# Kernel tuning notes

Hardware: AMD Instinct MI355X
Metric: run time of the kernel (lower is better)

## Reference

```python
import jax, jax.numpy as jnp
import numpy as np

FEATS = 64
H = FEATS * FEATS            # GRU hidden size = 4096
I = (FEATS + 1) * FEATS * 3  # GRU input size = 12480


def setup_inputs() -> dict:
    key = jax.random.key(0)
    ks = jax.random.split(key, 16)
    s = 0.02
    inp = {
        "data": jax.random.normal(ks[0], (FEATS, FEATS), dtype=jnp.float32),
        "hidden": jax.random.normal(ks[1], (1, 1, H), dtype=jnp.float32),
        # feature GAT params: fc (in=FEATS -> heads*out=FEATS*1, no fc bias in DGL GATConv)
        "fgat_W": jax.random.normal(ks[2], (FEATS, FEATS), dtype=jnp.float32) * s,
        "fgat_al": jax.random.normal(ks[3], (FEATS,), dtype=jnp.float32) * s,
        "fgat_ar": jax.random.normal(ks[4], (FEATS,), dtype=jnp.float32) * s,
        "fgat_b": jnp.zeros((FEATS,), dtype=jnp.float32),
        # time GAT params
        "tgat_W": jax.random.normal(ks[5], (FEATS, FEATS), dtype=jnp.float32) * s,
        "tgat_al": jax.random.normal(ks[6], (FEATS,), dtype=jnp.float32) * s,
        "tgat_ar": jax.random.normal(ks[7], (FEATS,), dtype=jnp.float32) * s,
        "tgat_b": jnp.zeros((FEATS,), dtype=jnp.float32),
        # GRU params (PyTorch layout: gates stacked [r, z, n])
        "W_ih": jax.random.normal(ks[8], (3 * H, I), dtype=jnp.float32) * s,
        "W_hh": jax.random.normal(ks[9], (3 * H, H), dtype=jnp.float32) * s,
        "b_ih": jnp.zeros((3 * H,), dtype=jnp.float32),
        "b_hh": jnp.zeros((3 * H,), dtype=jnp.float32),
    }
    return inp


def _gat_star(x, W, al, ar, b):
    """DGL GATConv(in=F, out=1, heads=F) on the star graph:
    edges src=1..F -> dst=0, plus self-loops on every node.
    x: (F+1, F). Returns (F+1, F) (out_feats=1 squeezed into head dim)."""
    h = x @ W                      # (N, heads) since out_feats == 1
    el = h * al                    # src attention logits per head
    er = h * ar                    # dst attention logits per head
    # Node 0 receives edges from every node (incl. its self-loop):
    e = jax.nn.leaky_relu(el + er[0], negative_slope=0.2)  # (N, heads)
    alpha = jax.nn.softmax(e, axis=0)
    out0 = jnp.sum(alpha * h, axis=0)                       # (heads,)
    # Nodes 1..F only have their self-loop -> softmax weight 1 -> out = h[v]
    out = h.at[0].set(out0) + b
    return out


def reference(data, hidden, fgat_W, fgat_al, fgat_ar, fgat_b,
              tgat_W, tgat_al, tgat_ar, tgat_b,
              W_ih, W_hh, b_ih, b_hh):
    F = FEATS
    d = data.reshape(F, F)
    zrow = jnp.zeros((1, F), dtype=d.dtype)

    data_r = jnp.concatenate([zrow, d], axis=0)        # (F+1, F)
    feat_r = _gat_star(data_r, fgat_W, fgat_al, fgat_ar, fgat_b)   # (F+1, F)

    data_t = jnp.concatenate([zrow, d.T], axis=0)      # (F+1, F)
    time_r = _gat_star(data_t, tgat_W, tgat_al, tgat_ar, tgat_b)   # (F+1, F)

    dd = data_r[..., None]                              # (F+1, F, 1)
    x = jnp.concatenate([dd, feat_r[..., None], time_r[..., None]], axis=2)
    x = x.reshape(-1)                                   # ((F+1)*F*3,)

    # single-step GRU (PyTorch gate math)
    h0 = hidden.reshape(-1)                             # (H,)
    gi = W_ih @ x + b_ih                                # (3H,)
    gh = W_hh @ h0 + b_hh                               # (3H,)
    r = jax.nn.sigmoid(gi[:H] + gh[:H])
    z = jax.nn.sigmoid(gi[H:2 * H] + gh[H:2 * H])
    n = jnp.tanh(gi[2 * H:] + r * gh[2 * H:])
    h_new = (1.0 - z) * n + z * h0                      # (H,)

    return (h_new, h_new.reshape(1, 1, H))
```

## Files before the change

### kernel.cpp

```cpp
#include <hip/hip_runtime.h>

#define FEATS 64
#define HSZ   4096
#define ISZ   12480
#define I4    (ISZ/4)
#define H4    (HSZ/4)

#define X_OFF  0
#define GI_OFF 12480
#define GH_OFF 24768

#define GI_RPW 4
#define GI_RPB 16
#define GH_RPW 12
#define GH_RPB 48
#define GI_NB  (3 * HSZ / GI_RPB)
#define GH_NB  (3 * HSZ / GH_RPB)

typedef float f4 __attribute__((ext_vector_type(4)));

__global__ __launch_bounds__(256)
void gat_fused(const float* __restrict__ data,
               const float* __restrict__ fW, const float* __restrict__ fal,
               const float* __restrict__ fb,
               const float* __restrict__ tW, const float* __restrict__ tal,
               const float* __restrict__ tb,
               float* __restrict__ ws) {
    __shared__ float ld[64][65];
    __shared__ float Wl[64][65];
    __shared__ float hb[64][65];
    __shared__ float out0[64];
    int w   = blockIdx.x;
    int tid = threadIdx.x;
    const float* W  = w ? tW  : fW;
    const float* al = w ? tal : fal;
    const float* bb = w ? tb  : fb;

    for (int i = tid; i < 4096; i += 256) {
        int r = i >> 6, c = i & 63;
        float v = data[i];
        if (w) ld[c][r] = v; else ld[r][c] = v;
        Wl[r][c] = W[i];
    }
    __syncthreads();

    {
        int vbase = (tid >> 6) * 16;
        int j     = tid & 63;
        float acc[16];
        #pragma unroll
        for (int v = 0; v < 16; ++v) acc[v] = 0.f;
        for (int k = 0; k < 64; ++k) {
            float wk = Wl[k][j];
            #pragma unroll
            for (int v = 0; v < 16; ++v)
                acc[v] = fmaf(ld[vbase + v][k], wk, acc[v]);
        }
        #pragma unroll
        for (int v = 0; v < 16; ++v) hb[vbase + v][j] = acc[v];
    }
    __syncthreads();

    if (tid < 64) {
        int j = tid;
        float a = al[j];
        float m = 0.f;
        for (int v = 0; v < 64; ++v) {
            float e = hb[v][j] * a;
            e = e > 0.f ? e : 0.2f * e;
            m = fmaxf(m, e);
        }
        float sum = __expf(0.f - m);
        float num = 0.f;
        for (int v = 0; v < 64; ++v) {
            float hv = hb[v][j];
            float e  = hv * a;
            e = e > 0.f ? e : 0.2f * e;
            float p  = __expf(e - m);
            sum += p;
            num += p * hv;
        }
        out0[j] = num / sum;
    }
    __syncthreads();

    for (int i = tid; i < 4160; i += 256) {
        int n = i >> 6, f = i & 63;
        float val = ((n == 0) ? out0[f] : hb[n - 1][f]) + bb[f];
        ws[X_OFF + i * 3 + 1 + w] = val;
        if (w == 0)
            ws[X_OFF + i * 3] = (n == 0) ? 0.f : data[(n - 1) * 64 + f];
    }
}

__device__ __forceinline__ float wave_reduce(float v) {
    #pragma unroll
    for (int off = 32; off > 0; off >>= 1) v += __shfl_down(v, off);
    return v;
}

__device__ __forceinline__ float fma4(f4 w, f4 v, float a) {
    return fmaf(w.x, v.x, fmaf(w.y, v.y, fmaf(w.z, v.z, fmaf(w.w, v.w, a))));
}

__device__ __forceinline__ f4 ntload(const f4* p) {
    return __builtin_nontemporal_load(p);
}

__global__ __launch_bounds__(256, 4)
void big_matvec(const float* __restrict__ W_ih,
                const float* __restrict__ W_hh,
                const float* __restrict__ h0,
                float* __restrict__ ws) {
    int b    = blockIdx.x;
    int wave = threadIdx.x >> 6;
    int lane = threadIdx.x & 63;

    if (b < GI_NB) {
        int r = b * GI_RPB + wave * GI_RPW;
        const f4* x4 = (const f4*)(ws + X_OFF);
        const f4* W0 = (const f4*)W_ih + (size_t)r * I4;
        const f4* W1 = W0 + I4;
        const f4* W2 = W1 + I4;
        const f4* W3 = W2 + I4;
        float a0 = 0.f, a1 = 0.f, a2 = 0.f, a3 = 0.f;
        int k = lane;
        #pragma unroll 4
        for (int i = 0; i < 48; ++i, k += 64) {
            f4 v = x4[k];
            a0 = fma4(ntload(W0 + k), v, a0);
            a1 = fma4(ntload(W1 + k), v, a1);
            a2 = fma4(ntload(W2 + k), v, a2);
            a3 = fma4(ntload(W3 + k), v, a3);
        }
        if (lane < 48) {
            int kk = 3072 + lane;
            f4 v = x4[kk];
            a0 = fma4(ntload(W0 + kk), v, a0);
            a1 = fma4(ntload(W1 + kk), v, a1);
            a2 = fma4(ntload(W2 + kk), v, a2);
            a3 = fma4(ntload(W3 + kk), v, a3);
        }
        a0 = wave_reduce(a0);
        a1 = wave_reduce(a1);
        a2 = wave_reduce(a2);
        a3 = wave_reduce(a3);
        if (lane == 0) {
            ws[GI_OFF + r]     = a0;
            ws[GI_OFF + r + 1] = a1;
            ws[GI_OFF + r + 2] = a2;
            ws[GI_OFF + r + 3] = a3;
        }
    } else {
        int base = (b - GI_NB) * GH_RPB + wave * GH_RPW;
        const f4* h4 = (const f4*)h0;
        #pragma unroll
        for (int p = 0; p < GH_RPW; p += 4) {
            int r = base + p;
            const f4* W0 = (const f4*)W_hh + (size_t)r * H4;
            const f4* W1 = W0 + H4;
            const f4* W2 = W1 + H4;
            const f4* W3 = W2 + H4;
            float a0 = 0.f, a1 = 0.f, a2 = 0.f, a3 = 0.f;
            int k = lane;
            #pragma unroll 4
            for (int i = 0; i < 16; ++i, k += 64) {
                f4 v = h4[k];
                a0 = fma4(ntload(W0 + k), v, a0);
                a1 = fma4(ntload(W1 + k), v, a1);
                a2 = fma4(ntload(W2 + k), v, a2);
                a3 = fma4(ntload(W3 + k), v, a3);
            }
            a0 = wave_reduce(a0);
            a1 = wave_reduce(a1);
            a2 = wave_reduce(a2);
            a3 = wave_reduce(a3);
            if (lane == 0) {
                ws[GH_OFF + r]     = a0;
                ws[GH_OFF + r + 1] = a1;
                ws[GH_OFF + r + 2] = a2;
                ws[GH_OFF + r + 3] = a3;
            }
        }
    }
}

__global__ void gru_combine(const float* __restrict__ h0,
                            const float* __restrict__ b_ih,
                            const float* __restrict__ b_hh,
                            const float* __restrict__ ws,
                            float* __restrict__ out) {
    int j = blockIdx.x * 256 + threadIdx.x;
    if (j >= HSZ) return;
    const float* gi = ws + GI_OFF;
    const float* gh = ws + GH_OFF;
    float ir  = gi[j]         + b_ih[j];
    float iz  = gi[HSZ + j]   + b_ih[HSZ + j];
    float in_ = gi[2*HSZ + j] + b_ih[2*HSZ + j];
    float hr  = gh[j]         + b_hh[j];
    float hz  = gh[HSZ + j]   + b_hh[HSZ + j];
    float hn  = gh[2*HSZ + j] + b_hh[2*HSZ + j];
    float r = 1.f / (1.f + expf(-(ir + hr)));
    float z = 1.f / (1.f + expf(-(iz + hz)));
    float n = tanhf(in_ + r * hn);
    float h = (1.f - z) * n + z * h0[j];
    out[j]       = h;
    out[HSZ + j] = h;
}

extern "C" void kernel_launch(void* const* d_in, const int* in_sizes, int n_in,
                              void* d_out, int out_size, void* d_ws, size_t ws_size,
                              hipStream_t stream) {
    const float* data    = (const float*)d_in[0];
    const float* hidden  = (const float*)d_in[1];
    const float* fgat_W  = (const float*)d_in[2];
    const float* fgat_al = (const float*)d_in[3];
    const float* fgat_b  = (const float*)d_in[5];
    const float* tgat_W  = (const float*)d_in[6];
    const float* tgat_al = (const float*)d_in[7];
    const float* tgat_b  = (const float*)d_in[9];
    const float* W_ih    = (const float*)d_in[10];
    const float* W_hh    = (const float*)d_in[11];
    const float* b_ih    = (const float*)d_in[12];
    const float* b_hh    = (const float*)d_in[13];
    float* ws  = (float*)d_ws;
    float* out = (float*)d_out;

    gat_fused<<<2, 256, 0, stream>>>(data, fgat_W, fgat_al, fgat_b,
                                     tgat_W, tgat_al, tgat_b, ws);
    big_matvec<<<GI_NB + GH_NB, 256, 0, stream>>>(W_ih, W_hh, hidden, ws);
    gru_combine<<<HSZ / 256, 256, 0, stream>>>(hidden, b_ih, b_hh, ws, out);
}
```

Baseline: 140.7 us.

## Fuse GAT, GRU matvecs and gate combine into one persistent kernel

Merges the three launches into a single 512-block kernel. Blocks 0-1 compute the GAT features and signal completion through an atomic counter, and every block computes its W_hh rows while that work runs. Each block then spins until x is ready, computes its W_ih rows, and the last block to finish (found with a second atomic) applies the GRU gate math. This removes launch gaps and overlaps the small GAT stage with the W_hh streaming. The cost is a memset launch, a spin-wait whose safety depends on blocks 0-1 being resident, and a serial combine done by only one block.

Measured after the change: 279.4 us. 98.6% more time.

```diff
diff --git a/kernel.cpp b/kernel.cpp
--- a/kernel.cpp
+++ b/kernel.cpp
@@ -6,206 +6,206 @@
 #define I4    (ISZ/4)
 #define H4    (HSZ/4)
 
-#define X_OFF  0
-#define GI_OFF 12480
-#define GH_OFF 24768
-
-#define GI_RPW 4
-#define GI_RPB 16
-#define GH_RPW 12
-#define GH_RPB 48
-#define GI_NB  (3 * HSZ / GI_RPB)
-#define GH_NB  (3 * HSZ / GH_RPB)
+#define X_OFF   0
+#define GI_OFF  12480
+#define GH_OFF  24768
+#define SYNC_OFF 37056
+
+#define NBLK 512
+#define RPB  24
+#define RPW  6
 
 typedef float f4 __attribute__((ext_vector_type(4)));
 
-__global__ __launch_bounds__(256)
-void gat_fused(const float* __restrict__ data,
-               const float* __restrict__ fW, const float* __restrict__ fal,
-               const float* __restrict__ fb,
-               const float* __restrict__ tW, const float* __restrict__ tal,
-               const float* __restrict__ tb,
-               float* __restrict__ ws) {
-    __shared__ float ld[64][65];
-    __shared__ float Wl[64][65];
+__device__ __forceinline__ float wave_reduce(float v) {
+    #pragma unroll
+    for (int off = 32; off > 0; off >>= 1) v += __shfl_down(v, off);
+    return v;
+}
+
+__device__ __forceinline__ float fma4(f4 w, f4 v, float a) {
+    return fmaf(w.x, v.x, fmaf(w.y, v.y, fmaf(w.z, v.z, fmaf(w.w, v.w, a))));
+}
+
+__device__ __forceinline__ f4 ntload(const f4* p) {
+    return __builtin_nontemporal_load(p);
+}
+
+__global__ __launch_bounds__(256, 2)
+void mega(const float* __restrict__ data,
+          const float* __restrict__ fW, const float* __restrict__ fal,
+          const float* __restrict__ fb,
+          const float* __restrict__ tW, const float* __restrict__ tal,
+          const float* __restrict__ tb,
+          const float* __restrict__ W_ih, const float* __restrict__ W_hh,
+          const float* __restrict__ h0,
+          const float* __restrict__ b_ih, const float* __restrict__ b_hh,
+          float* __restrict__ ws, float* __restrict__ out) {
     __shared__ float hb[64][65];
     __shared__ float out0[64];
-    int w   = blockIdx.x;
-    int tid = threadIdx.x;
-    const float* W  = w ? tW  : fW;
-    const float* al = w ? tal : fal;
-    const float* bb = w ? tb  : fb;
-
-    for (int i = tid; i < 4096; i += 256) {
-        int r = i >> 6, c = i & 63;
-        float v = data[i];
-        if (w) ld[c][r] = v; else ld[r][c] = v;
-        Wl[r][c] = W[i];
-    }
-    __syncthreads();
-
-    {
-        int vbase = (tid >> 6) * 16;
-        int j     = tid & 63;
+    __shared__ int   sLast;
+    int b = blockIdx.x, tid = threadIdx.x;
+    int wave = tid >> 6, lane = tid & 63;
+    int* sync = (int*)(ws + SYNC_OFF);
+
+    if (b < 2) {
+        const float* Wg = b ? tW  : fW;
+        const float* al = b ? tal : fal;
+        const float* bb = b ? tb  : fb;
+        int vbase = wave * 16, j = lane;
         float acc[16];
         #pragma unroll
         for (int v = 0; v < 16; ++v) acc[v] = 0.f;
         for (int k = 0; k < 64; ++k) {
-            float wk = Wl[k][j];
+            float wk = Wg[k * 64 + j];
             #pragma unroll
-            for (int v = 0; v < 16; ++v)
-                acc[v] = fmaf(ld[vbase + v][k], wk, acc[v]);
+            for (int v = 0; v < 16; ++v) {
+                float dv = b ? data[k * 64 + vbase + v]
+                             : data[(vbase + v) * 64 + k];
+                acc[v] = fmaf(dv, wk, acc[v]);
+            }
         }
         #pragma unroll
         for (int v = 0; v < 16; ++v) hb[vbase + v][j] = acc[v];
+        __syncthreads();
+
+        if (tid < 64) {
+            int j2 = tid;
+            float a = al[j2];
+            float m = 0.f;
+            for (int v = 0; v < 64; ++v) {
+                float e = hb[v][j2] * a;
+                e = e > 0.f ? e : 0.2f * e;
+                m = fmaxf(m, e);
+            }
+            float sum = __expf(0.f - m);
+            float num = 0.f;
+            for (int v = 0; v < 64; ++v) {
+                float hv = hb[v][j2];
+                float e  = hv * a;
+                e = e > 0.f ? e : 0.2f * e;
+                float p  = __expf(e - m);
+                sum += p;
+                num += p * hv;
+            }
+            out0[j2] = num / sum;
+        }
+        __syncthreads();
+
+        for (int i = tid; i < 4160; i += 256) {
+            int n = i >> 6, f = i & 63;
+            float val = ((n == 0) ? out0[f] : hb[n - 1][f]) + bb[f];
+            ws[X_OFF + i * 3 + 1 + b] = val;
+            if (b == 0)
+                ws[X_OFF + i * 3] = (n == 0) ? 0.f : data[(n - 1) * 64 + f];
+        }
+        __syncthreads();
+        __threadfence();
+        if (tid == 0)
+            __hip_atomic_fetch_add(sync, 1, __ATOMIC_RELEASE,
+                                   __HIP_MEMORY_SCOPE_AGENT);
+    }
+
+    {
+        int r = b * RPB + wave * RPW;
+        const f4* h4 = (const f4*)h0;
+        const f4* Wb = (const f4*)W_hh + (size_t)r * H4;
+        float a0 = 0.f, a1 = 0.f, a2 = 0.f, a3 = 0.f, a4 = 0.f, a5 = 0.f;
+        int k = lane;
+        #pragma unroll 2
+        for (int i = 0; i < 16; ++i, k += 64) {
+            f4 v = h4[k];
+            a0 = fma4(ntload(Wb + k),          v, a0);
+            a1 = fma4(ntload(Wb + H4 + k),     v, a1);
+            a2 = fma4(ntload(Wb + 2 * H4 + k), v, a2);
+            a3 = fma4(ntload(Wb + 3 * H4 + k), v, a3);
+            a4 = fma4(ntload(Wb + 4 * H4 + k), v, a4);
+            a5 = fma4(ntload(Wb + 5 * H4 + k), v, a5);
+        }
+        a0 = wave_reduce(a0); a1 = wave_reduce(a1); a2 = wave_reduce(a2);
+        a3 = wave_reduce(a3); a4 = wave_reduce(a4); a5 = wave_reduce(a5);
+        if (lane == 0) {
+            ws[GH_OFF + r]     = a0 + b_hh[r];
+            ws[GH_OFF + r + 1] = a1 + b_hh[r + 1];
+            ws[GH_OFF + r + 2] = a2 + b_hh[r + 2];
+            ws[GH_OFF + r + 3] = a3 + b_hh[r + 3];
+            ws[GH_OFF + r + 4] = a4 + b_hh[r + 4];
+            ws[GH_OFF + r + 5] = a5 + b_hh[r + 5];
+        }
+    }
+
+    if (tid == 0) {
+        while (__hip_atomic_load(sync, __ATOMIC_RELAXED,
+                                 __HIP_MEMORY_SCOPE_AGENT) < 2)
+            __builtin_amdgcn_s_sleep(8);
     }
     __syncthreads();
-
-    if (tid < 64) {
-        int j = tid;
-        float a = al[j];
-        float m = 0.f;
-        for (int v = 0; v < 64; ++v) {
-            float e = hb[v][j] * a;
-            e = e > 0.f ? e : 0.2f * e;
-            m = fmaxf(m, e);
-        }
-        float sum = __expf(0.f - m);
-        float num = 0.f;
-        for (int v = 0; v < 64; ++v) {
-            float hv = hb[v][j];
-            float e  = hv * a;
-            e = e > 0.f ? e : 0.2f * e;
-            float p  = __expf(e - m);
-            sum += p;
-            num += p * hv;
-        }
-        out0[j] = num / sum;
-    }
-    __syncthreads();
-
-    for (int i = tid; i < 4160; i += 256) {
-        int n = i >> 6, f = i & 63;
-        float val = ((n == 0) ? out0[f] : hb[n - 1][f]) + bb[f];
-        ws[X_OFF + i * 3 + 1 + w] = val;
-        if (w == 0)
-            ws[X_OFF + i * 3] = (n == 0) ? 0.f : data[(n - 1) * 64 + f];
-    }
-}
-
-__device__ __forceinline__ float wave_reduce(float v) {
-    #pragma unroll
-    for (int off = 32; off > 0; off >>= 1) v += __shfl_down(v, off);
-    return v;
-}
-
-__device__ __forceinline__ float fma4(f4 w, f4 v, float a) {
-    return fmaf(w.x, v.x, fmaf(w.y, v.y, fmaf(w.z, v.z, fmaf(w.w, v.w, a))));
-}
-
-__device__ __forceinline__ f4 ntload(const f4* p) {
-    return __builtin_nontemporal_load(p);
-}
-
-__global__ __launch_bounds__(256, 4)
-void big_matvec(const float* __restrict__ W_ih,
-                const float* __restrict__ W_hh,
-                const float* __restrict__ h0,
-                float* __restrict__ ws) {
-    int b    = blockIdx.x;
-    int wave = threadIdx.x >> 6;
-    int lane = threadIdx.x & 63;
-
-    if (b < GI_NB) {
-        int r = b * GI_RPB + wave * GI_RPW;
+    __threadfence();
+
+    {
+        int r = b * RPB + wave * RPW;
         const f4* x4 = (const f4*)(ws + X_OFF);
-        const f4* W0 = (const f4*)W_ih + (size_t)r * I4;
-        const f4* W1 = W0 + I4;
-        const f4* W2 = W1 + I4;
-        const f4* W3 = W2 + I4;
-        float a0 = 0.f, a1 = 0.f, a2 = 0.f, a3 = 0.f;
+        const f4* Wb = (const f4*)W_ih + (size_t)r * I4;
+        float a0 = 0.f, a1 = 0.f, a2 = 0.f, a3 = 0.f, a4 = 0.f, a5 = 0.f;
         int k = lane;
-        #pragma unroll 4
+        #pragma unroll 2
         for (int i = 0; i < 48; ++i, k += 64) {
             f4 v = x4[k];
-            a0 = fma4(ntload(W0 + k), v, a0);
-            a1 = fma4(ntload(W1 + k), v, a1);
-            a2 = fma4(ntload(W2 + k), v, a2);
-            a3 = fma4(ntload(W3 + k), v, a3);
+            a0 = fma4(ntload(Wb + k),          v, a0);
+            a1 = fma4(ntload(Wb + I4 + k),     v, a1);
+            a2 = fma4(ntload(Wb + 2 * I4 + k), v, a2);
+            a3 = fma4(ntload(Wb + 3 * I4 + k), v, a3);
+            a4 = fma4(ntload(Wb + 4 * I4 + k), v, a4);
+            a5 = fma4(ntload(Wb + 5 * I4 + k), v, a5);
         }
         if (lane < 48) {
             int kk = 3072 + lane;
             f4 v = x4[kk];
-            a0 = fma4(ntload(W0 + kk), v, a0);
-            a1 = fma4(ntload(W1 + kk), v, a1);
-            a2 = fma4(ntload(W2 + kk), v, a2);
-            a3 = fma4(ntload(W3 + kk), v, a3);
-        }
-        a0 = wave_reduce(a0);
-        a1 = wave_reduce(a1);
-        a2 = wave_reduce(a2);
-        a3 = wave_reduce(a3);
+            a0 = fma4(ntload(Wb + kk),          v, a0);
+            a1 = fma4(ntload(Wb + I4 + kk),     v, a1);
+            a2 = fma4(ntload(Wb + 2 * I4 + kk), v, a2);
+            a3 = fma4(ntload(Wb + 3 * I4 + kk), v, a3);
+            a4 = fma4(ntload(Wb + 4 * I4 + kk), v, a4);
+            a5 = fma4(ntload(Wb + 5 * I4 + kk), v, a5);
+        }
+        a0 = wave_reduce(a0); a1 = wave_reduce(a1); a2 = wave_reduce(a2);
+        a3 = wave_reduce(a3); a4 = wave_reduce(a4); a5 = wave_reduce(a5);
         if (lane == 0) {
-            ws[GI_OFF + r]     = a0;
-            ws[GI_OFF + r + 1] = a1;
-            ws[GI_OFF + r + 2] = a2;
-            ws[GI_OFF + r + 3] = a3;
-        }
-    } else {
-        int base = (b - GI_NB) * GH_RPB + wave * GH_RPW;
-        const f4* h4 = (const f4*)h0;
+            ws[GI_OFF + r]     = a0 + b_ih[r];
+            ws[GI_OFF + r + 1] = a1 + b_ih[r + 1];
+            ws[GI_OFF + r + 2] = a2 + b_ih[r + 2];
+            ws[GI_OFF + r + 3] = a3 + b_ih[r + 3];
+            ws[GI_OFF + r + 4] = a4 + b_ih[r + 4];
+            ws[GI_OFF + r + 5] = a5 + b_ih[r + 5];
+        }
+    }
+
+    __threadfence();
+    if (tid == 0) {
+        int old = __hip_atomic_fetch_add(sync + 1, 1, __ATOMIC_ACQ_REL,
+                                         __HIP_MEMORY_SCOPE_AGENT);
+        sLast = (old == NBLK - 1);
+    }
+    __syncthreads();
+    if (sLast) {
+        __threadfence();
         #pragma unroll
-        for (int p = 0; p < GH_RPW; p += 4) {
-            int r = base + p;
-            const f4* W0 = (const f4*)W_hh + (size_t)r * H4;
-            const f4* W1 = W0 + H4;
-            const f4* W2 = W1 + H4;
-            const f4* W3 = W2 + H4;
-            float a0 = 0.f, a1 = 0.f, a2 = 0.f, a3 = 0.f;
-            int k = lane;
-            #pragma unroll 4
-            for (int i = 0; i < 16; ++i, k += 64) {
-                f4 v = h4[k];
-                a0 = fma4(ntload(W0 + k), v, a0);
-                a1 = fma4(ntload(W1 + k), v, a1);
-                a2 = fma4(ntload(W2 + k), v, a2);
-                a3 = fma4(ntload(W3 + k), v, a3);
-            }
-            a0 = wave_reduce(a0);
-            a1 = wave_reduce(a1);
-            a2 = wave_reduce(a2);
-            a3 = wave_reduce(a3);
-            if (lane == 0) {
-                ws[GH_OFF + r]     = a0;
-                ws[GH_OFF + r + 1] = a1;
-                ws[GH_OFF + r + 2] = a2;
-                ws[GH_OFF + r + 3] = a3;
-            }
-        }
-    }
-}
-
-__global__ void gru_combine(const float* __restrict__ h0,
-                            const float* __restrict__ b_ih,
-                            const float* __restrict__ b_hh,
-                            const float* __restrict__ ws,
-                            float* __restrict__ out) {
-    int j = blockIdx.x * 256 + threadIdx.x;
-    if (j >= HSZ) return;
-    const float* gi = ws + GI_OFF;
-    const float* gh = ws + GH_OFF;
-    float ir  = gi[j]         + b_ih[j];
-    float iz  = gi[HSZ + j]   + b_ih[HSZ + j];
-    float in_ = gi[2*HSZ + j] + b_ih[2*HSZ + j];
-    float hr  = gh[j]         + b_hh[j];
-    float hz  = gh[HSZ + j]   + b_hh[HSZ + j];
-    float hn  = gh[2*HSZ + j] + b_hh[2*HSZ + j];
-    float r = 1.f / (1.f + expf(-(ir + hr)));
-    float z = 1.f / (1.f + expf(-(iz + hz)));
-    float n = tanhf(in_ + r * hn);
-    float h = (1.f - z) * n + z * h0[j];
-    out[j]       = h;
-    out[HSZ + j] = h;
+        for (int t = 0; t < 16; ++t) {
+            int j = t * 256 + tid;
+            float ir  = ws[GI_OFF + j];
+            float iz  = ws[GI_OFF + HSZ + j];
+            float in_ = ws[GI_OFF + 2 * HSZ + j];
+            float hr  = ws[GH_OFF + j];
+            float hz  = ws[GH_OFF + HSZ + j];
+            float hn  = ws[GH_OFF + 2 * HSZ + j];
+            float r = 1.f / (1.f + __expf(-(ir + hr)));
+            float z = 1.f / (1.f + __expf(-(iz + hz)));
+            float n = tanhf(in_ + r * hn);
+            float h = (1.f - z) * n + z * h0[j];
+            out[j]       = h;
+            out[HSZ + j] = h;
+        }
+    }
 }
 
 extern "C" void kernel_launch(void* const* d_in, const int* in_sizes, int n_in,
@@ -226,8 +226,9 @@
     float* ws  = (float*)d_ws;
     float* out = (float*)d_out;
 
-    gat_fused<<<2, 256, 0, stream>>>(data, fgat_W, fgat_al, fgat_b,
-                                     tgat_W, tgat_al, tgat_b, ws);
-    big_matvec<<<GI_NB + GH_NB, 256, 0, stream>>>(W_ih, W_hh, hidden, ws);
-    gru_combine<<<HSZ / 256, 256, 0, stream>>>(hidden, b_ih, b_hh, ws, out);
-}
+    hipMemsetAsync((char*)d_ws + SYNC_OFF * sizeof(float), 0, 2 * sizeof(int),
+                   stream);
+    mega<<<NBLK, 256, 0, stream>>>(data, fgat_W, fgat_al, fgat_b,
+                                   tgat_W, tgat_al, tgat_b,
+                                   W_ih, W_hh, hidden, b_ih, b_hh, ws, out);
+}
```

## Fuse GRU combine into matvec via last-block atomic and split GAT over 8 blocks

Applied to the files above, without the earlier changes.

Removes the separate gru_combine launch. Each matvec block adds its bias, bumps an atomic counter in the workspace, and the last block to finish computes the GRU gates for all 4096 outputs. The GAT kernel is split from 2 blocks into 8, each handling 16 output heads, to shorten the serial front stage. This adds a memset launch to reset the counter. It also makes the final elementwise pass run serially on a single block.

Measured after the change: 368.4 us. 2.62x slower.

```diff
diff --git a/kernel.cpp b/kernel.cpp
--- a/kernel.cpp
+++ b/kernel.cpp
@@ -6,9 +6,10 @@
 #define I4    (ISZ/4)
 #define H4    (HSZ/4)
 
-#define X_OFF  0
-#define GI_OFF 12480
-#define GH_OFF 24768
+#define X_OFF    0
+#define GI_OFF   12480
+#define GH_OFF   24768
+#define SYNC_OFF 37056
 
 #define GI_RPW 4
 #define GI_RPB 16
@@ -16,23 +17,25 @@
 #define GH_RPB 48
 #define GI_NB  (3 * HSZ / GI_RPB)
 #define GH_NB  (3 * HSZ / GH_RPB)
+#define NBLK   (GI_NB + GH_NB)
 
 typedef float f4 __attribute__((ext_vector_type(4)));
 
 __global__ __launch_bounds__(256)
-void gat_fused(const float* __restrict__ data,
-               const float* __restrict__ fW, const float* __restrict__ fal,
-               const float* __restrict__ fb,
-               const float* __restrict__ tW, const float* __restrict__ tal,
-               const float* __restrict__ tb,
-               float* __restrict__ ws) {
+void gat8(const float* __restrict__ data,
+          const float* __restrict__ fW, const float* __restrict__ fal,
+          const float* __restrict__ fb,
+          const float* __restrict__ tW, const float* __restrict__ tal,
+          const float* __restrict__ tb,
+          float* __restrict__ ws) {
     __shared__ float ld[64][65];
-    __shared__ float Wl[64][65];
-    __shared__ float hb[64][65];
-    __shared__ float out0[64];
-    int w   = blockIdx.x;
+    __shared__ float Wl[64][17];
+    __shared__ float hb[64][17];
+    __shared__ float out0[16];
+    int b = blockIdx.x;
+    int w = b >> 2, q = b & 3;
     int tid = threadIdx.x;
-    const float* W  = w ? tW  : fW;
+    const float* Wg = w ? tW  : fW;
     const float* al = w ? tal : fal;
     const float* bb = w ? tb  : fb;
 
@@ -40,56 +43,61 @@
         int r = i >> 6, c = i & 63;
         float v = data[i];
         if (w) ld[c][r] = v; else ld[r][c] = v;
-        Wl[r][c] = W[i];
+    }
+    for (int i = tid; i < 1024; i += 256) {
+        int k = i >> 4, jj = i & 15;
+        Wl[k][jj] = Wg[k * 64 + q * 16 + jj];
     }
     __syncthreads();
 
     {
-        int vbase = (tid >> 6) * 16;
-        int j     = tid & 63;
-        float acc[16];
-        #pragma unroll
-        for (int v = 0; v < 16; ++v) acc[v] = 0.f;
+        int v = tid & 63, jr = tid >> 6;
+        float a0 = 0.f, a1 = 0.f, a2 = 0.f, a3 = 0.f;
+        #pragma unroll 8
         for (int k = 0; k < 64; ++k) {
-            float wk = Wl[k][j];
-            #pragma unroll
-            for (int v = 0; v < 16; ++v)
-                acc[v] = fmaf(ld[vbase + v][k], wk, acc[v]);
-        }
-        #pragma unroll
-        for (int v = 0; v < 16; ++v) hb[vbase + v][j] = acc[v];
-    }
-    __syncthreads();
-
-    if (tid < 64) {
-        int j = tid;
-        float a = al[j];
+            float dv = ld[v][k];
+            a0 = fmaf(dv, Wl[k][jr * 4 + 0], a0);
+            a1 = fmaf(dv, Wl[k][jr * 4 + 1], a1);
+            a2 = fmaf(dv, Wl[k][jr * 4 + 2], a2);
+            a3 = fmaf(dv, Wl[k][jr * 4 + 3], a3);
+        }
+        hb[v][jr * 4 + 0] = a0;
+        hb[v][jr * 4 + 1] = a1;
+        hb[v][jr * 4 + 2] = a2;
+        hb[v][jr * 4 + 3] = a3;
+    }
+    __syncthreads();
+
+    if (tid < 16) {
+        int jj = tid;
+        float a = al[q * 16 + jj];
         float m = 0.f;
         for (int v = 0; v < 64; ++v) {
-            float e = hb[v][j] * a;
+            float e = hb[v][jj] * a;
             e = e > 0.f ? e : 0.2f * e;
             m = fmaxf(m, e);
         }
         float sum = __expf(0.f - m);
         float num = 0.f;
         for (int v = 0; v < 64; ++v) {
-            float hv = hb[v][j];
+            float hv = hb[v][jj];
             float e  = hv * a;
             e = e > 0.f ? e : 0.2f * e;
             float p  = __expf(e - m);
             sum += p;
             num += p * hv;
         }
-        out0[j] = num / sum;
-    }
-    __syncthreads();
-
-    for (int i = tid; i < 4160; i += 256) {
-        int n = i >> 6, f = i & 63;
-        float val = ((n == 0) ? out0[f] : hb[n - 1][f]) + bb[f];
-        ws[X_OFF + i * 3 + 1 + w] = val;
+        out0[jj] = num / sum;
+    }
+    __syncthreads();
+
+    for (int i = tid; i < 1040; i += 256) {
+        int n = i >> 4, ff = i & 15;
+        int f = q * 16 + ff;
+        float val = ((n == 0) ? out0[ff] : hb[n - 1][ff]) + bb[f];
+        ws[X_OFF + (n * 64 + f) * 3 + 1 + w] = val;
         if (w == 0)
-            ws[X_OFF + i * 3] = (n == 0) ? 0.f : data[(n - 1) * 64 + f];
+            ws[X_OFF + (n * 64 + f) * 3] = (n == 0) ? 0.f : ld[n - 1][f];
     }
 }
 
@@ -111,10 +119,15 @@
 void big_matvec(const float* __restrict__ W_ih,
                 const float* __restrict__ W_hh,
                 const float* __restrict__ h0,
-                float* __restrict__ ws) {
+                const float* __restrict__ b_ih,
+                const float* __restrict__ b_hh,
+                float* __restrict__ ws,
+                float* __restrict__ out) {
+    __shared__ int sLast;
     int b    = blockIdx.x;
-    int wave = threadIdx.x >> 6;
-    int lane = threadIdx.x & 63;
+    int tid  = threadIdx.x;
+    int wave = tid >> 6;
+    int lane = tid & 63;
 
     if (b < GI_NB) {
         int r = b * GI_RPB + wave * GI_RPW;
@@ -146,10 +159,10 @@
         a2 = wave_reduce(a2);
         a3 = wave_reduce(a3);
         if (lane == 0) {
-            ws[GI_OFF + r]     = a0;
-            ws[GI_OFF + r + 1] = a1;
-            ws[GI_OFF + r + 2] = a2;
-            ws[GI_OFF + r + 3] = a3;
+            ws[GI_OFF + r]     = a0 + b_ih[r];
+            ws[GI_OFF + r + 1] = a1 + b_ih[r + 1];
+            ws[GI_OFF + r + 2] = a2 + b_ih[r + 2];
+            ws[GI_OFF + r + 3] = a3 + b_ih[r + 3];
         }
     } else {
         int base = (b - GI_NB) * GH_RPB + wave * GH_RPW;
@@ -176,36 +189,41 @@
             a2 = wave_reduce(a2);
             a3 = wave_reduce(a3);
             if (lane == 0) {
-                ws[GH_OFF + r]     = a0;
-                ws[GH_OFF + r + 1] = a1;
-                ws[GH_OFF + r + 2] = a2;
-                ws[GH_OFF + r + 3] = a3;
+                ws[GH_OFF + r]     = a0 + b_hh[r];
+                ws[GH_OFF + r + 1] = a1 + b_hh[r + 1];
+                ws[GH_OFF + r + 2] = a2 + b_hh[r + 2];
+                ws[GH_OFF + r + 3] = a3 + b_hh[r + 3];
             }
         }
     }
-}
-
-__global__ void gru_combine(const float* __restrict__ h0,
-                            const float* __restrict__ b_ih,
-                            const float* __restrict__ b_hh,
-                            const float* __restrict__ ws,
-                            float* __restrict__ out) {
-    int j = blockIdx.x * 256 + threadIdx.x;
-    if (j >= HSZ) return;
-    const float* gi = ws + GI_OFF;
-    const float* gh = ws + GH_OFF;
-    float ir  = gi[j]         + b_ih[j];
-    float iz  = gi[HSZ + j]   + b_ih[HSZ + j];
-    float in_ = gi[2*HSZ + j] + b_ih[2*HSZ + j];
-    float hr  = gh[j]         + b_hh[j];
-    float hz  = gh[HSZ + j]   + b_hh[HSZ + j];
-    float hn  = gh[2*HSZ + j] + b_hh[2*HSZ + j];
-    float r = 1.f / (1.f + expf(-(ir + hr)));
-    float z = 1.f / (1.f + expf(-(iz + hz)));
-    float n = tanhf(in_ + r * hn);
-    float h = (1.f - z) * n + z * h0[j];
-    out[j]       = h;
-    out[HSZ + j] = h;
+
+    __threadfence();
+    if (tid == 0) {
+        int old = __hip_atomic_fetch_add((int*)(ws + SYNC_OFF), 1,
+                                         __ATOMIC_ACQ_REL,
+                                         __HIP_MEMORY_SCOPE_AGENT);
+        sLast = (old == NBLK - 1);
+    }
+    __syncthreads();
+    if (sLast) {
+        __threadfence();
+        #pragma unroll
+        for (int t = 0; t < 16; ++t) {
+            int j = t * 256 + tid;
+            float ir  = ws[GI_OFF + j];
+            float iz  = ws[GI_OFF + HSZ + j];
+            float in_ = ws[GI_OFF + 2 * HSZ + j];
+            float hr  = ws[GH_OFF + j];
+            float hz  = ws[GH_OFF + HSZ + j];
+            float hn  = ws[GH_OFF + 2 * HSZ + j];
+            float r = 1.f / (1.f + __expf(-(ir + hr)));
+            float z = 1.f / (1.f + __expf(-(iz + hz)));
+            float n = tanhf(in_ + r * hn);
+            float h = (1.f - z) * n + z * h0[j];
+            out[j]       = h;
+            out[HSZ + j] = h;
+        }
+    }
 }
 
 extern "C" void kernel_launch(void* const* d_in, const int* in_sizes, int n_in,
@@ -226,8 +244,8 @@
     float* ws  = (float*)d_ws;
     float* out = (float*)d_out;
 
-    gat_fused<<<2, 256, 0, stream>>>(data, fgat_W, fgat_al, fgat_b,
-                                     tgat_W, tgat_al, tgat_b, ws);
-    big_matvec<<<GI_NB + GH_NB, 256, 0, stream>>>(W_ih, W_hh, hidden, ws);
-    gru_combine<<<HSZ / 256, 256, 0, stream>>>(hidden, b_ih, b_hh, ws, out);
-}
+    hipMemsetAsync((char*)d_ws + SYNC_OFF * sizeof(float), 0, sizeof(int), stream);
+    gat8<<<8, 256, 0, stream>>>(data, fgat_W, fgat_al, fgat_b,
+                                tgat_W, tgat_al, tgat_b, ws);
+    big_matvec<<<NBLK, 256, 0, stream>>>(W_ih, W_hh, hidden, b_ih, b_hh, ws, out);
+}
```
